# Performance work log

Measured on AMD Instinct MI355X. Metric: run time of the kernel, lower is better.

The kernel has to match this reference:

```python
import jax, jax.numpy as jnp
import numpy as np

N_NODES = 100000


def _degrees(src, dst, n):
    ones = jnp.ones(src.shape[0], dtype=jnp.float32)
    deg_out = jax.ops.segment_sum(ones, src, num_segments=n)
    deg_in = jax.ops.segment_sum(ones, dst, num_segments=n)
    # DGL clamps degrees to min 1 before pow(-0.5)
    return jnp.clip(deg_out, 1.0) ** -0.5, jnp.clip(deg_in, 1.0) ** -0.5


def _graph_conv(x, src, dst, W, b, norm_out, norm_in, n):
    # norm='both': scale source by D_out^-1/2, aggregate (copy_u + sum), scale dest by D_in^-1/2
    # weight applied before aggregation (in_feats >= out_feats for all layers; math-equivalent)
    h = (x * norm_out[:, None]) @ W                      # [N, out]
    agg = jax.ops.segment_sum(h[src], dst, num_segments=n)  # SpMM via gather+scatter-add
    return agg * norm_in[:, None] + b


def setup_inputs() -> dict:
    key = jax.random.key(0)
    ks = jax.random.split(key, 8)
    E = 1600000
    return {
        "in_feat": jax.random.normal(ks[0], (N_NODES, 128), dtype=jnp.float32),
        "src": jax.random.randint(ks[1], (E,), 0, N_NODES),
        "dst": jax.random.randint(ks[2], (E,), 0, N_NODES),
        "W1": jax.random.normal(ks[3], (128, 128), dtype=jnp.float32) * (128 ** -0.5),
        "b1": jnp.zeros((128,), dtype=jnp.float32),
        "W2": jax.random.normal(ks[4], (128, 128), dtype=jnp.float32) * (128 ** -0.5),
        "b2": jnp.zeros((128,), dtype=jnp.float32),
        "W3": jax.random.normal(ks[5], (128, 64), dtype=jnp.float32) * (128 ** -0.5),
        "b3": jnp.zeros((64,), dtype=jnp.float32),
    }


def reference(in_feat, src, dst, W1, b1, W2, b2, W3, b3):
    n = in_feat.shape[0]
    norm_out, norm_in = _degrees(src, dst, n)
    h = jax.nn.relu(_graph_conv(in_feat, src, dst, W1, b1, norm_out, norm_in, n))
    h = jax.nn.relu(_graph_conv(h, src, dst, W2, b2, norm_out, norm_in, n))
    h = _graph_conv(h, src, dst, W3, b3, norm_out, norm_in, n)
    return h
```

## Files before the change

kernel.cpp:

```cpp
#include <hip/hip_runtime.h>

#define THREADS 256
#define SCAN_BLK 1024
#define NR 8
#define NC 32

typedef __attribute__((ext_vector_type(8))) short short8;
typedef __attribute__((ext_vector_type(4))) float floatx4;

__device__ __forceinline__ ushort f2bf(float f) {
    union { float f; uint u; } v; v.f = f;
    uint u = v.u;
    return (ushort)((u + 0x7FFFu + ((u >> 16) & 1u)) >> 16);
}
__device__ __forceinline__ float bf_lo(uint u) {
    union { uint u; float f; } v; v.u = u << 16; return v.f;
}
__device__ __forceinline__ float bf_hi(uint u) {
    union { uint u; float f; } v; v.u = u & 0xFFFF0000u; return v.f;
}

__global__ __launch_bounds__(256) void k1_kernel(const int* __restrict__ dst,
                                                 int* __restrict__ cnt_in,
                                                 int* __restrict__ rank, int E) {
    int t = blockIdx.x * blockDim.x + threadIdx.x;
    int e0 = t * 4;
    if (e0 + 4 <= E) {
        int4 d4 = *(const int4*)(dst + e0);
        int4 r;
        r.x = atomicAdd(&cnt_in[d4.x], 1);
        r.y = atomicAdd(&cnt_in[d4.y], 1);
        r.z = atomicAdd(&cnt_in[d4.z], 1);
        r.w = atomicAdd(&cnt_in[d4.w], 1);
        *(int4*)(rank + e0) = r;
    } else if (e0 < E) {
        for (int e = e0; e < E; ++e) rank[e] = atomicAdd(&cnt_in[dst[e]], 1);
    }
}

__global__ __launch_bounds__(256) void hist_out_kernel(const int* __restrict__ src,
                                                       int* __restrict__ cnt_out,
                                                       int n, int E) {
    __shared__ uint cnt[12544];
    const int range = blockIdx.x / NC;
    const int chunk = blockIdx.x % NC;
    const int Rsz = (n + NR - 1) / NR;
    const int lo  = range * Rsz;
    const int R   = min(n - lo, Rsz);
    if (R <= 0) return;
    for (int i = threadIdx.x; i < R; i += THREADS) cnt[i] = 0;
    __syncthreads();

    const int per = (E + NC - 1) / NC;
    const int c0 = chunk * per;
    const int c1 = min(E, c0 + per);
    int i = c0 + threadIdx.x * 4;
    for (; i + 4 <= c1; i += THREADS * 4) {
        int4 v = *(const int4*)(src + i);
        if ((unsigned)(v.x - lo) < (unsigned)R) atomicAdd(&cnt[v.x - lo], 1u);
        if ((unsigned)(v.y - lo) < (unsigned)R) atomicAdd(&cnt[v.y - lo], 1u);
        if ((unsigned)(v.z - lo) < (unsigned)R) atomicAdd(&cnt[v.z - lo], 1u);
        if ((unsigned)(v.w - lo) < (unsigned)R) atomicAdd(&cnt[v.w - lo], 1u);
    }
    for (; i < c1; ++i) {
        int s = src[i];
        if ((unsigned)(s - lo) < (unsigned)R) atomicAdd(&cnt[s - lo], 1u);
    }
    __syncthreads();
    for (int k = threadIdx.x; k < R; k += THREADS) {
        uint c = cnt[k];
        if (c) atomicAdd(&cnt_out[lo + k], (int)c);
    }
}

__global__ void scan_phase1(const int* __restrict__ cnt, int* __restrict__ blk_sums, int n) {
    int base = blockIdx.x * SCAN_BLK;
    int t = threadIdx.x;
    int sum = 0;
    for (int i = t; i < SCAN_BLK; i += THREADS) {
        int idx = base + i;
        sum += (idx < n) ? cnt[idx] : 0;
    }
    __shared__ int wsum[4];
    for (int off = 32; off > 0; off >>= 1) sum += __shfl_down(sum, off);
    if ((t & 63) == 0) wsum[t >> 6] = sum;
    __syncthreads();
    if (t == 0) blk_sums[blockIdx.x] = wsum[0] + wsum[1] + wsum[2] + wsum[3];
}

__global__ void scan_phase2(int* __restrict__ blk_sums, int nb) {
    __shared__ int s[1024];
    int t = threadIdx.x;
    s[t] = (t < nb) ? blk_sums[t] : 0;
    __syncthreads();
    for (int off = 1; off < 1024; off <<= 1) {
        int v = s[t];
        if (t >= off) v += s[t - off];
        __syncthreads();
        s[t] = v;
        __syncthreads();
    }
    if (t < nb) blk_sums[t] = (t == 0) ? 0 : s[t - 1];
}

__global__ void scan_phase3(const int* __restrict__ cnt, const int* __restrict__ cnt_out,
                            const int* __restrict__ blk_sums,
                            int* __restrict__ row_off, float* __restrict__ norm_in,
                            float* __restrict__ norm_out, int n, int E) {
    __shared__ int ts[THREADS];
    int b = blockIdx.x, t = threadIdx.x;
    int base = b * SCAN_BLK + t * 4;
    int local[4], val[4]; int s = 0;
    #pragma unroll
    for (int k = 0; k < 4; ++k) {
        local[k] = s;
        int idx = base + k;
        int v = (idx < n) ? cnt[idx] : 0;
        val[k] = v;
        s += v;
    }
    ts[t] = s;
    __syncthreads();
    for (int off = 1; off < THREADS; off <<= 1) {
        int v = ts[t];
        if (t >= off) v += ts[t - off];
        __syncthreads();
        ts[t] = v;
        __syncthreads();
    }
    int excl = (t == 0) ? 0 : ts[t - 1];
    int boff = blk_sums[b];
    #pragma unroll
    for (int k = 0; k < 4; ++k) {
        int idx = base + k;
        if (idx < n) {
            row_off[idx] = boff + excl + local[k];
            norm_in[idx]  = rsqrtf((float)max(val[k], 1));
            norm_out[idx] = rsqrtf((float)max(cnt_out[idx], 1));
        }
    }
    if (b == 0 && t == 0) row_off[n] = E;
}

__global__ void fill2_kernel(const int* __restrict__ src, const int* __restrict__ dst,
                             const int* __restrict__ rank, const int* __restrict__ row_off,
                             int* __restrict__ csr_src, int E) {
    int t = blockIdx.x * blockDim.x + threadIdx.x;
    int e0 = t * 4;
    if (e0 + 4 <= E) {
        int4 s4 = *(const int4*)(src + e0);
        int4 d4 = *(const int4*)(dst + e0);
        int4 r4 = *(const int4*)(rank + e0);
        csr_src[row_off[d4.x] + r4.x] = s4.x;
        csr_src[row_off[d4.y] + r4.y] = s4.y;
        csr_src[row_off[d4.z] + r4.z] = s4.z;
        csr_src[row_off[d4.w] + r4.w] = s4.w;
    } else if (e0 < E) {
        for (int e = e0; e < E; ++e) csr_src[row_off[dst[e]] + rank[e]] = src[e];
    }
}

__device__ __forceinline__ void wpack_one(const float* __restrict__ W, ushort* __restrict__ Wpk,
                                          int OUT, int t) {
    int lane = t & 63, kk = (t >> 6) & 3, ct = t >> 8;
    int col = ct * 16 + (lane & 15);
    int k0 = kk * 32 + (lane >> 4) * 8;
    #pragma unroll
    for (int j = 0; j < 8; ++j)
        Wpk[t * 8 + j] = f2bf(W[(size_t)(k0 + j) * OUT + col]);
}

__global__ void wpack_all(const float* __restrict__ W1, const float* __restrict__ W2,
                          const float* __restrict__ W3, ushort* __restrict__ Wpk1,
                          ushort* __restrict__ Wpk2, ushort* __restrict__ Wpk3) {
    int t = blockIdx.x * blockDim.x + threadIdx.x;
    if (t < 2048)      wpack_one(W1, Wpk1, 128, t);
    else if (t < 4096) wpack_one(W2, Wpk2, 128, t - 2048);
    else if (t < 5120) wpack_one(W3, Wpk3, 64,  t - 4096);
}

template<int OUT, bool IN_F32>
__global__ __launch_bounds__(256) void mfma_gemm(const void* __restrict__ xv,
                                                 const ushort* __restrict__ Wpk,
                                                 const float* __restrict__ norm,
                                                 ushort* __restrict__ h, int n) {
    __shared__ ushort xs[64 * 136];
    const int t = threadIdx.x;
    const int row0 = blockIdx.x * 64;

    if (IN_F32) {
        const float* x = (const float*)xv;
        #pragma unroll
        for (int i = 0; i < 8; ++i) {
            int e = (i * 256 + t) * 4;
            int row = e >> 7, col = e & 127;
            int gr = min(row0 + row, n - 1);
            float nf = norm[gr];
            float4 v = *(const float4*)(x + (size_t)gr * 128 + col);
            ushort4 p;
            p.x = f2bf(v.x * nf); p.y = f2bf(v.y * nf);
            p.z = f2bf(v.z * nf); p.w = f2bf(v.w * nf);
            *(ushort4*)(&xs[row * 136 + col]) = p;
        }
    } else {
        const ushort* x = (const ushort*)xv;
        #pragma unroll
        for (int i = 0; i < 4; ++i) {
            int e = (i * 256 + t) * 8;
            int row = e >> 7, col = e & 127;
            int gr = min(row0 + row, n - 1);
            float nf = norm[gr];
            uint4 v = *(const uint4*)(x + (size_t)gr * 128 + col);
            uint4 o;
            o.x = f2bf(bf_lo(v.x) * nf) | ((uint)f2bf(bf_hi(v.x) * nf) << 16);
            o.y = f2bf(bf_lo(v.y) * nf) | ((uint)f2bf(bf_hi(v.y) * nf) << 16);
            o.z = f2bf(bf_lo(v.z) * nf) | ((uint)f2bf(bf_hi(v.z) * nf) << 16);
            o.w = f2bf(bf_lo(v.w) * nf) | ((uint)f2bf(bf_hi(v.w) * nf) << 16);
            *(uint4*)(&xs[row * 136 + col]) = o;
        }
    }
    __syncthreads();

    const int wave = t >> 6, lane = t & 63;
    const int r = lane & 15, g = lane >> 4;
    const int nrow0 = row0 + wave * 16;

    short8 a[4];
    #pragma unroll
    for (int kk = 0; kk < 4; ++kk)
        a[kk] = *(const short8*)(&xs[(wave * 16 + r) * 136 + kk * 32 + g * 8]);

    const short8* wp = (const short8*)Wpk;
    #pragma unroll
    for (int ct = 0; ct < OUT / 16; ++ct) {
        floatx4 acc = {0.f, 0.f, 0.f, 0.f};
        #pragma unroll
        for (int kk = 0; kk < 4; ++kk) {
            short8 b = wp[(ct * 4 + kk) * 64 + lane];
            acc = __builtin_amdgcn_mfma_f32_16x16x32_bf16(a[kk], b, acc, 0, 0, 0);
        }
        int col = ct * 16 + r;
        #pragma unroll
        for (int rr = 0; rr < 4; ++rr) {
            int grow = nrow0 + g * 4 + rr;
            if (grow < n) h[(size_t)grow * OUT + col] = f2bf(acc[rr]);
        }
    }
}

template<bool RELU>
__global__ __launch_bounds__(256) void agg128(const ushort* __restrict__ h,
                                              const int* __restrict__ row_off,
                                              const int* __restrict__ csr_src,
                                              const float* __restrict__ nin,
                                              const float* __restrict__ bias,
                                              ushort* __restrict__ out, int n) {
    const int wave = threadIdx.x >> 6;
    const int lane = threadIdx.x & 63;
    const uint* hu = (const uint*)h;
    for (int node = blockIdx.x * 4 + wave; node < n; node += gridDim.x * 4) {
        int beg = row_off[node], end = row_off[node + 1];
        float a0 = 0.f, a1 = 0.f;
        int j = beg;
        for (; j + 3 < end; j += 4) {
            int s0 = csr_src[j], s1 = csr_src[j + 1], s2 = csr_src[j + 2], s3 = csr_src[j + 3];
            uint u0 = hu[(size_t)s0 * 64 + lane];
            uint u1 = hu[(size_t)s1 * 64 + lane];
            uint u2 = hu[(size_t)s2 * 64 + lane];
            uint u3 = hu[(size_t)s3 * 64 + lane];
            a0 += bf_lo(u0); a1 += bf_hi(u0);
            a0 += bf_lo(u1); a1 += bf_hi(u1);
            a0 += bf_lo(u2); a1 += bf_hi(u2);
            a0 += bf_lo(u3); a1 += bf_hi(u3);
        }
        for (; j < end; ++j) {
            uint u = hu[(size_t)csr_src[j] * 64 + lane];
            a0 += bf_lo(u); a1 += bf_hi(u);
        }
        float nf = nin[node];
        float2 bb = *(const float2*)(bias + 2 * lane);
        float r0 = a0 * nf + bb.x;
        float r1 = a1 * nf + bb.y;
        if (RELU) { r0 = fmaxf(r0, 0.f); r1 = fmaxf(r1, 0.f); }
        ((uint*)out)[(size_t)node * 64 + lane] = (uint)f2bf(r0) | ((uint)f2bf(r1) << 16);
    }
}

__global__ __launch_bounds__(256) void agg64_final(const ushort* __restrict__ h,
                                                   const int* __restrict__ row_off,
                                                   const int* __restrict__ csr_src,
                                                   const float* __restrict__ nin,
                                                   const float* __restrict__ bias,
                                                   float* __restrict__ out, int n) {
    const int wave = threadIdx.x >> 6;
    const int lane = threadIdx.x & 63;
    const int half = lane >> 5, u5 = lane & 31;
    const uint* hu = (const uint*)h;
    for (int node = blockIdx.x * 4 + wave; node < n; node += gridDim.x * 4) {
        int beg = row_off[node], end = row_off[node + 1];
        float a0 = 0.f, a1 = 0.f;
        int j = beg + half;
        for (; j + 2 < end; j += 4) {
            int sA = csr_src[j], sB = csr_src[j + 2];
            uint uA = hu[(size_t)sA * 32 + u5];
            uint uB = hu[(size_t)sB * 32 + u5];
            a0 += bf_lo(uA); a1 += bf_hi(uA);
            a0 += bf_lo(uB); a1 += bf_hi(uB);
        }
        if (j < end) {
            uint u = hu[(size_t)csr_src[j] * 32 + u5];
            a0 += bf_lo(u); a1 += bf_hi(u);
        }
        float o0 = a0 + __shfl(a0, u5 + 32);
        float o1 = a1 + __shfl(a1, u5 + 32);
        if (lane < 32) {
            float nf = nin[node];
            float2 bb = *(const float2*)(bias + 2 * u5);
            float2 r;
            r.x = o0 * nf + bb.x;
            r.y = o1 * nf + bb.y;
            *(float2*)(out + (size_t)node * 64 + 2 * u5) = r;
        }
    }
}

extern "C" void kernel_launch(void* const* d_in, const int* in_sizes, int n_in,
                              void* d_out, int out_size, void* d_ws, size_t ws_size,
                              hipStream_t stream) {
    const float* in_feat = (const float*)d_in[0];
    const int*   src     = (const int*)d_in[1];
    const int*   dst     = (const int*)d_in[2];
    const float* W1      = (const float*)d_in[3];
    const float* b1      = (const float*)d_in[4];
    const float* W2      = (const float*)d_in[5];
    const float* b2      = (const float*)d_in[6];
    const float* W3      = (const float*)d_in[7];
    const float* b3      = (const float*)d_in[8];

    const int n = in_sizes[0] / 128;
    const int E = in_sizes[1];
    float* out = (float*)d_out;

    float* ws       = (float*)d_ws;
    float* norm_out = ws;
    float* norm_in  = ws + n;
    int*   row_off  = (int*)(ws + 2 * (size_t)n);
    int*   csr_src  = row_off + (n + 2);
    ushort* Wpk1    = (ushort*)(csr_src + E);
    ushort* Wpk2    = Wpk1 + 128 * 128;
    ushort* Wpk3    = Wpk2 + 128 * 128;
    ushort* bufA    = Wpk3 + 128 * 64;
    ushort* bufB    = bufA + (size_t)n * 128;
    int* cnt_in   = (int*)bufA;
    int* cnt_out  = cnt_in + n;
    int* blk_sums = cnt_out + n;
    int* rank     = (int*)bufB;

    const int nb = (n + SCAN_BLK - 1) / SCAN_BLK;

    hipMemsetAsync(cnt_in, 0, 2 * (size_t)n * sizeof(int), stream);
    wpack_all<<<20, THREADS, 0, stream>>>(W1, W2, W3, Wpk1, Wpk2, Wpk3);
    k1_kernel<<<(E / 4 + THREADS - 1) / THREADS, THREADS, 0, stream>>>(dst, cnt_in, rank, E);
    hist_out_kernel<<<NR * NC, THREADS, 0, stream>>>(src, cnt_out, n, E);
    scan_phase1<<<nb, THREADS, 0, stream>>>(cnt_in, blk_sums, n);
    scan_phase2<<<1, 1024, 0, stream>>>(blk_sums, nb);
    scan_phase3<<<nb, THREADS, 0, stream>>>(cnt_in, cnt_out, blk_sums, row_off, norm_in, norm_out, n, E);
    fill2_kernel<<<(E / 4 + THREADS - 1) / THREADS, THREADS, 0, stream>>>(src, dst, rank, row_off, csr_src, E);

    const int gemm_grid = (n + 63) / 64;
    const int agg_grid  = 4096;

    mfma_gemm<128, true><<<gemm_grid, THREADS, 0, stream>>>(in_feat, Wpk1, norm_out, bufA, n);
    agg128<true><<<agg_grid, THREADS, 0, stream>>>(bufA, row_off, csr_src, norm_in, b1, bufB, n);
    mfma_gemm<128, false><<<gemm_grid, THREADS, 0, stream>>>(bufB, Wpk2, norm_out, bufA, n);
    agg128<true><<<agg_grid, THREADS, 0, stream>>>(bufA, row_off, csr_src, norm_in, b2, bufB, n);
    mfma_gemm<64, false><<<gemm_grid, THREADS, 0, stream>>>(bufB, Wpk3, norm_out, bufA, n);
    agg64_final<<<agg_grid, THREADS, 0, stream>>>(bufA, row_off, csr_src, norm_in, b3, out, n);
}
```

Before: 433.5 us.

## Build CSR via range-partitioned LDS counting sort instead of global atomics

Replaces the global-atomic in-degree count with per-rank bookkeeping, and the scattered fill pass, with a three-phase partitioned counting sort. Each block counts a node range over an edge chunk in shared memory using packed 16-bit counters, then column sums and per-chunk bases are computed, and a final pass places edges using LDS atomic cursors. The aim is to replace contended global atomics and random rank/row_off reads with shared-memory atomics. In exchange it adds extra kernels, a large partial-count buffer, and uses only NR*NC=256 blocks, which may under-occupy the GPU; edges within a row are no longer in input order.

```diff
diff --git a/kernel.cpp b/kernel.cpp
--- a/kernel.cpp
+++ b/kernel.cpp
@@ -4,6 +4,7 @@
 #define SCAN_BLK 1024
 #define NR 8
 #define NC 32
+#define RSTRIDE 12544
 
 typedef __attribute__((ext_vector_type(8))) short short8;
 typedef __attribute__((ext_vector_type(4))) float floatx4;
@@ -20,37 +21,18 @@
     union { uint u; float f; } v; v.u = u & 0xFFFF0000u; return v.f;
 }
 
-__global__ __launch_bounds__(256) void k1_kernel(const int* __restrict__ dst,
-                                                 int* __restrict__ cnt_in,
-                                                 int* __restrict__ rank, int E) {
-    int t = blockIdx.x * blockDim.x + threadIdx.x;
-    int e0 = t * 4;
-    if (e0 + 4 <= E) {
-        int4 d4 = *(const int4*)(dst + e0);
-        int4 r;
-        r.x = atomicAdd(&cnt_in[d4.x], 1);
-        r.y = atomicAdd(&cnt_in[d4.y], 1);
-        r.z = atomicAdd(&cnt_in[d4.z], 1);
-        r.w = atomicAdd(&cnt_in[d4.w], 1);
-        *(int4*)(rank + e0) = r;
-    } else if (e0 < E) {
-        for (int e = e0; e < E; ++e) rank[e] = atomicAdd(&cnt_in[dst[e]], 1);
-    }
-}
-
 __global__ __launch_bounds__(256) void hist_out_kernel(const int* __restrict__ src,
                                                        int* __restrict__ cnt_out,
                                                        int n, int E) {
-    __shared__ uint cnt[12544];
-    const int range = blockIdx.x / NC;
-    const int chunk = blockIdx.x % NC;
+    __shared__ uint cnt[RSTRIDE];
+    const int range = blockIdx.x % NR;
+    const int chunk = blockIdx.x / NR;
     const int Rsz = (n + NR - 1) / NR;
     const int lo  = range * Rsz;
     const int R   = min(n - lo, Rsz);
     if (R <= 0) return;
     for (int i = threadIdx.x; i < R; i += THREADS) cnt[i] = 0;
     __syncthreads();
-
     const int per = (E + NC - 1) / NC;
     const int c0 = chunk * per;
     const int c1 = min(E, c0 + per);
@@ -62,14 +44,115 @@
         if ((unsigned)(v.z - lo) < (unsigned)R) atomicAdd(&cnt[v.z - lo], 1u);
         if ((unsigned)(v.w - lo) < (unsigned)R) atomicAdd(&cnt[v.w - lo], 1u);
     }
-    for (; i < c1; ++i) {
-        int s = src[i];
-        if ((unsigned)(s - lo) < (unsigned)R) atomicAdd(&cnt[s - lo], 1u);
+    if (i < c1) {
+        for (int e = i; e < c1 && e < i + 4; ++e) {
+            int s = src[e];
+            if ((unsigned)(s - lo) < (unsigned)R) atomicAdd(&cnt[s - lo], 1u);
+        }
     }
     __syncthreads();
     for (int k = threadIdx.x; k < R; k += THREADS) {
         uint c = cnt[k];
         if (c) atomicAdd(&cnt_out[lo + k], (int)c);
+    }
+}
+
+__global__ __launch_bounds__(256) void csr_phaseA(const int* __restrict__ dst,
+                                                  ushort* __restrict__ PC, int n, int E) {
+    __shared__ uint cnt[RSTRIDE / 2];
+    const int range = blockIdx.x % NR;
+    const int chunk = blockIdx.x / NR;
+    const int Rsz = (n + NR - 1) / NR;
+    const int lo  = range * Rsz;
+    const int R   = min(n - lo, Rsz);
+    if (R <= 0) return;
+    const int Rp = (R + 2) >> 1;
+    for (int i = threadIdx.x; i < Rp; i += THREADS) cnt[i] = 0;
+    __syncthreads();
+    const int per = (E + NC - 1) / NC;
+    const int c0 = chunk * per;
+    const int c1 = min(E, c0 + per);
+    int i = c0 + threadIdx.x * 4;
+    for (; i + 4 <= c1; i += THREADS * 4) {
+        int4 v = *(const int4*)(dst + i);
+        int kx = v.x - lo, ky = v.y - lo, kz = v.z - lo, kw = v.w - lo;
+        if ((unsigned)kx < (unsigned)R) atomicAdd(&cnt[kx >> 1], (kx & 1) ? 65536u : 1u);
+        if ((unsigned)ky < (unsigned)R) atomicAdd(&cnt[ky >> 1], (ky & 1) ? 65536u : 1u);
+        if ((unsigned)kz < (unsigned)R) atomicAdd(&cnt[kz >> 1], (kz & 1) ? 65536u : 1u);
+        if ((unsigned)kw < (unsigned)R) atomicAdd(&cnt[kw >> 1], (kw & 1) ? 65536u : 1u);
+    }
+    if (i < c1) {
+        for (int e = i; e < c1 && e < i + 4; ++e) {
+            int k = dst[e] - lo;
+            if ((unsigned)k < (unsigned)R) atomicAdd(&cnt[k >> 1], (k & 1) ? 65536u : 1u);
+        }
+    }
+    __syncthreads();
+    ushort* pc = PC + (size_t)(range * NC + chunk) * RSTRIDE;
+    for (int k = threadIdx.x; k < R; k += THREADS) {
+        uint c = cnt[k >> 1];
+        pc[k] = (ushort)((k & 1) ? (c >> 16) : (c & 0xFFFFu));
+    }
+}
+
+__global__ void csr_colsum(const ushort* __restrict__ PC, int* __restrict__ cnt_in, int n) {
+    int gk = blockIdx.x * blockDim.x + threadIdx.x;
+    if (gk >= n) return;
+    const int Rsz = (n + NR - 1) / NR;
+    int r = gk / Rsz, k = gk - r * Rsz;
+    int t = 0;
+    #pragma unroll 4
+    for (int c = 0; c < NC; ++c)
+        t += PC[(size_t)(r * NC + c) * RSTRIDE + k];
+    cnt_in[gk] = t;
+}
+
+__global__ void csr_mkbase(const ushort* __restrict__ PC, const int* __restrict__ row_off,
+                           int* __restrict__ B, int n) {
+    int gk = blockIdx.x * blockDim.x + threadIdx.x;
+    if (gk >= n) return;
+    const int Rsz = (n + NR - 1) / NR;
+    int r = gk / Rsz, k = gk - r * Rsz;
+    int base = row_off[gk];
+    for (int c = 0; c < NC; ++c) {
+        size_t idx = (size_t)(r * NC + c) * RSTRIDE + k;
+        B[idx] = base;
+        base += PC[idx];
+    }
+}
+
+__global__ __launch_bounds__(256) void csr_phaseC(const int* __restrict__ src,
+                                                  const int* __restrict__ dst,
+                                                  const int* __restrict__ B,
+                                                  int* __restrict__ csr_src, int n, int E) {
+    __shared__ int cur[RSTRIDE];
+    const int range = blockIdx.x % NR;
+    const int chunk = blockIdx.x / NR;
+    const int Rsz = (n + NR - 1) / NR;
+    const int lo  = range * Rsz;
+    const int R   = min(n - lo, Rsz);
+    if (R <= 0) return;
+    const int* b = B + (size_t)(range * NC + chunk) * RSTRIDE;
+    for (int i = threadIdx.x; i < R; i += THREADS) cur[i] = b[i];
+    __syncthreads();
+    const int per = (E + NC - 1) / NC;
+    const int c0 = chunk * per;
+    const int c1 = min(E, c0 + per);
+    int i = c0 + threadIdx.x * 4;
+    for (; i + 4 <= c1; i += THREADS * 4) {
+        int4 d = *(const int4*)(dst + i);
+        int4 s = *(const int4*)(src + i);
+        int kx = d.x - lo, ky = d.y - lo, kz = d.z - lo, kw = d.w - lo;
+        if ((unsigned)kx < (unsigned)R) csr_src[atomicAdd(&cur[kx], 1)] = s.x;
+        if ((unsigned)ky < (unsigned)R) csr_src[atomicAdd(&cur[ky], 1)] = s.y;
+        if ((unsigned)kz < (unsigned)R) csr_src[atomicAdd(&cur[kz], 1)] = s.z;
+        if ((unsigned)kw < (unsigned)R) csr_src[atomicAdd(&cur[kw], 1)] = s.w;
+    }
+    if (i < c1) {
+        for (int e = i; e < c1 && e < i + 4; ++e) {
+            int k = dst[e] - lo;
+            if ((unsigned)k < (unsigned)R) csr_src[atomicAdd(&cur[k], 1)] = src[e];
+        }
     }
 }
 
@@ -140,24 +223,6 @@
         }
     }
     if (b == 0 && t == 0) row_off[n] = E;
-}
-
-__global__ void fill2_kernel(const int* __restrict__ src, const int* __restrict__ dst,
-                             const int* __restrict__ rank, const int* __restrict__ row_off,
-                             int* __restrict__ csr_src, int E) {
-    int t = blockIdx.x * blockDim.x + threadIdx.x;
-    int e0 = t * 4;
-    if (e0 + 4 <= E) {
-        int4 s4 = *(const int4*)(src + e0);
-        int4 d4 = *(const int4*)(dst + e0);
-        int4 r4 = *(const int4*)(rank + e0);
-        csr_src[row_off[d4.x] + r4.x] = s4.x;
-        csr_src[row_off[d4.y] + r4.y] = s4.y;
-        csr_src[row_off[d4.z] + r4.z] = s4.z;
-        csr_src[row_off[d4.w] + r4.w] = s4.w;
-    } else if (e0 < E) {
-        for (int e = e0; e < E; ++e) csr_src[row_off[dst[e]] + rank[e]] = src[e];
-    }
 }
 
 __device__ __forceinline__ void wpack_one(const float* __restrict__ W, ushort* __restrict__ Wpk,
@@ -345,27 +410,30 @@
     float* norm_out = ws;
     float* norm_in  = ws + n;
     int*   row_off  = (int*)(ws + 2 * (size_t)n);
-    int*   csr_src  = row_off + (n + 2);
+    int*   csr_src  = row_off + (n + 4);
     ushort* Wpk1    = (ushort*)(csr_src + E);
     ushort* Wpk2    = Wpk1 + 128 * 128;
     ushort* Wpk3    = Wpk2 + 128 * 128;
     ushort* bufA    = Wpk3 + 128 * 64;
     ushort* bufB    = bufA + (size_t)n * 128;
-    int* cnt_in   = (int*)bufA;
-    int* cnt_out  = cnt_in + n;
-    int* blk_sums = cnt_out + n;
-    int* rank     = (int*)bufB;
+    int*    cnt_in   = (int*)bufA;
+    int*    cnt_out  = cnt_in + n;
+    int*    blk_sums = cnt_out + n;
+    ushort* PC       = (ushort*)(blk_sums + 128);
+    int*    Bbase    = (int*)(PC + (size_t)NR * NC * RSTRIDE);
 
     const int nb = (n + SCAN_BLK - 1) / SCAN_BLK;
 
-    hipMemsetAsync(cnt_in, 0, 2 * (size_t)n * sizeof(int), stream);
+    hipMemsetAsync(cnt_out, 0, (size_t)n * sizeof(int), stream);
     wpack_all<<<20, THREADS, 0, stream>>>(W1, W2, W3, Wpk1, Wpk2, Wpk3);
-    k1_kernel<<<(E / 4 + THREADS - 1) / THREADS, THREADS, 0, stream>>>(dst, cnt_in, rank, E);
     hist_out_kernel<<<NR * NC, THREADS, 0, stream>>>(src, cnt_out, n, E);
+    csr_phaseA<<<NR * NC, THREADS, 0, stream>>>(dst, PC, n, E);
+    csr_colsum<<<(n + THREADS - 1) / THREADS, THREADS, 0, stream>>>(PC, cnt_in, n);
     scan_phase1<<<nb, THREADS, 0, stream>>>(cnt_in, blk_sums, n);
     scan_phase2<<<1, 1024, 0, stream>>>(blk_sums, nb);
     scan_phase3<<<nb, THREADS, 0, stream>>>(cnt_in, cnt_out, blk_sums, row_off, norm_in, norm_out, n, E);
-    fill2_kernel<<<(E / 4 + THREADS - 1) / THREADS, THREADS, 0, stream>>>(src, dst, rank, row_off, csr_src, E);
+    csr_mkbase<<<(n + THREADS - 1) / THREADS, THREADS, 0, stream>>>(PC, row_off, Bbase, n);
+    csr_phaseC<<<NR * NC, THREADS, 0, stream>>>(src, dst, Bbase, csr_src, n, E);
 
     const int gemm_grid = (n + 63) / 64;
     const int agg_grid  = 4096;
```

New measurement: 417.4 us. 3.7% less time.
